# Kernel optimization log

Hardware: AMD Instinct MI355X
Metric: run time of the kernel (lower is better)

Reference implementation:

```python
import jax, jax.numpy as jnp
from jax import lax
import numpy as np

RADIUS = 0.1
NSAMPLE = 32
STRIDE = 3
ED_NSAMPLE = 10


def _sqdist(a, b):
    # a: [B,M,3], b: [B,N,3] -> [B,M,N] squared euclidean distance
    return (jnp.sum(a * a, -1)[:, :, None] + jnp.sum(b * b, -1)[:, None, :]
            - 2.0 * jnp.einsum('bmc,bnc->bmn', a, b))


def setup_inputs() -> dict:
    key = jax.random.key(0)
    ks = jax.random.split(key, 16)
    B, N = 8, 4096
    s = 0.05
    inp = {
        'data': jax.random.normal(ks[0], (B, N, 3), dtype=jnp.float32),
        'numpoints': N,
        # stem MLP 3 -> 64
        'W_stem': jax.random.normal(ks[1], (3, 64), dtype=jnp.float32) * s,
        'b_stem': jnp.zeros((64,), jnp.float32),
        # SA shared MLP (3 dp + 64 fj) -> 128
        'W_sa': jax.random.normal(ks[2], (67, 128), dtype=jnp.float32) * s,
        'b_sa': jnp.zeros((128,), jnp.float32),
        # FP MLP (128 interp + 64 skip) -> 64
        'W_fp': jax.random.normal(ks[3], (192, 64), dtype=jnp.float32) * s,
        'b_fp': jnp.zeros((64,), jnp.float32),
        # eigen-feature MLP 3 -> 4 -> 4
        'W_e1': jax.random.normal(ks[4], (3, 4), dtype=jnp.float32) * s,
        'b_e1': jnp.zeros((4,), jnp.float32),
        'W_e2': jax.random.normal(ks[5], (4, 4), dtype=jnp.float32) * s,
        'b_e2': jnp.zeros((4,), jnp.float32),
        # conv_final 1x1: 68 -> 64, + BN affine
        'W_fin': jax.random.normal(ks[6], (68, 64), dtype=jnp.float32) * s,
        'b_fin': jnp.zeros((64,), jnp.float32),
        'gamma': jnp.ones((64,), jnp.float32),
        'beta': jnp.zeros((64,), jnp.float32),
    }
    return inp


def reference(data, numpoints, W_stem, b_stem, W_sa, b_sa, W_fp, b_fp,
              W_e1, b_e1, W_e2, b_e2, W_fin, b_fin, gamma, beta):
    B, N, _ = data.shape
    b_ix = jnp.arange(B)[:, None, None]

    # ---------- encoder: stem MLP ----------
    f0 = jax.nn.relu(data @ W_stem + b_stem)  # [B,N,64]

    # set abstraction: stride-subsample centers, ball query, dp_fj, MLP, max
    sub_idx = jnp.arange(0, N, STRIDE)
    new_xyz = data[:, sub_idx]                 # [B,M,3]
    d2 = _sqdist(new_xyz, data)                # [B,M,N]
    col = jnp.arange(N, dtype=jnp.int32)
    valid = d2 < RADIUS * RADIUS
    keys = jnp.where(valid, col, N + col)      # first-valid ball query ordering
    negk, _ = lax.top_k(-keys, NSAMPLE)
    idx = -negk                                # [B,M,ns]
    first = idx[..., :1]                       # self point always valid
    idx = jnp.where(idx >= N, first, idx)
    g_xyz = data[b_ix, idx]                    # [B,M,ns,3]
    dp = (g_xyz - new_xyz[:, :, None, :]) / RADIUS  # normalize_dp
    g_f = f0[b_ix, idx]                        # [B,M,ns,64]
    feat = jnp.concatenate([dp, g_f], -1)      # [B,M,ns,67]
    h = jax.nn.relu(feat @ W_sa + b_sa)        # [B,M,ns,128]
    f_sub = jnp.max(h, axis=2)                 # [B,M,128]

    # ---------- decoder: 3-NN inverse-distance feature propagation ----------
    d2f = _sqdist(data, new_xyz)               # [B,N,M]
    negd, nn = lax.top_k(-d2f, 3)
    w = 1.0 / (-negd + 1e-8)
    w = w / jnp.sum(w, -1, keepdims=True)      # [B,N,3]
    nbr_f = f_sub[b_ix, nn]                    # [B,N,3,128]
    interp = jnp.einsum('bnk,bnkc->bnc', w, nbr_f)
    f = jax.nn.relu(jnp.concatenate([interp, f0], -1) @ W_fp + b_fp)  # [B,N,64]

    # ---------- KNN covariance eigen-features ----------
    d2e = _sqdist(data, data)                  # [B,N,N]
    _, gidx = lax.top_k(-d2e, ED_NSAMPLE)      # [B,N,k]
    nbr = data[b_ix, gidx]                     # [B,N,k,3]
    cen = nbr - jnp.mean(nbr, axis=2, keepdims=True)
    cov = jnp.einsum('bnkc,bnkd->bncd', cen, cen) / ED_NSAMPLE  # [B,N,3,3]
    eig = jnp.linalg.eigvalsh(cov)             # [B,N,3] ascending
    ef = jax.nn.relu(eig @ W_e1 + b_e1) @ W_e2 + b_e2  # [B,N,4]

    # ---------- fused 1x1 conv + BN (training-mode stats) + relu ----------
    z_in = jnp.concatenate([f, ef], -1)        # [B,N,68]
    zc = z_in @ W_fin + b_fin                  # [B,N,64]
    mu = jnp.mean(zc, axis=(0, 1))
    var = jnp.var(zc, axis=(0, 1))
    z = jax.nn.relu((zc - mu) * lax.rsqrt(var + 1e-5) * gamma + beta)
    z = jnp.transpose(z, (0, 2, 1))            # [B,64,N]
    return (data, z)
```

## Files before the change

kernel.cpp:

```cpp
#include <hip/hip_runtime.h>
#include <stdint.h>

#define BB 8
#define NN 4096
#define MM 1366
#define NS 32
#define RAD2 0.01f
#define NCH 16
#define CHUNK (NN/NCH)

static_assert(NCH * CHUNK == NN, "chunking");

__device__ __forceinline__ float rl(float v, int l) {
    return __int_as_float(__builtin_amdgcn_readlane(__float_as_int(v), l));
}
__device__ __forceinline__ uint32_t um(uint32_t a, uint32_t b) { return a < b ? a : b; }
__device__ __forceinline__ uint32_t ux(uint32_t a, uint32_t b) { return a > b ? a : b; }
__device__ __forceinline__ uint32_t um3(uint32_t a, uint32_t b, uint32_t c) { return um(um(a, b), c); }

__device__ __forceinline__ void mrg2(uint32_t* kk, uint32_t s0, uint32_t s1) {
    uint32_t n0 = um(kk[0], s0);
    uint32_t n1 = um3(kk[1], ux(kk[0], s0), s1);
    uint32_t n2 = um3(kk[2], ux(kk[1], s0), ux(kk[0], s1));
    uint32_t n3 = um3(kk[3], ux(kk[2], s0), ux(kk[1], s1));
    uint32_t n4 = um3(kk[4], ux(kk[3], s0), ux(kk[2], s1));
    uint32_t n5 = um3(kk[5], ux(kk[4], s0), ux(kk[3], s1));
    uint32_t n6 = um3(kk[6], ux(kk[5], s0), ux(kk[4], s1));
    uint32_t n7 = um3(kk[7], ux(kk[6], s0), ux(kk[5], s1));
    uint32_t n8 = um3(kk[8], ux(kk[7], s0), ux(kk[6], s1));
    uint32_t n9 = um3(kk[9], ux(kk[8], s0), ux(kk[7], s1));
    kk[0]=n0; kk[1]=n1; kk[2]=n2; kk[3]=n3; kk[4]=n4;
    kk[5]=n5; kk[6]=n6; kk[7]=n7; kk[8]=n8; kk[9]=n9;
}

__device__ __forceinline__ void mrg4(uint32_t* kk, uint32_t s0, uint32_t s1,
                                     uint32_t s2, uint32_t s3) {
    uint32_t n0 = um(kk[0], s0);
    uint32_t n1 = um3(kk[1], ux(kk[0], s0), s1);
    uint32_t n2 = um(um3(kk[2], ux(kk[1], s0), ux(kk[0], s1)), s2);
    uint32_t n3 = um3(um3(kk[3], ux(kk[2], s0), ux(kk[1], s1)), ux(kk[0], s2), s3);
    uint32_t n4 = um3(um3(kk[4], ux(kk[3], s0), ux(kk[2], s1)), ux(kk[1], s2), ux(kk[0], s3));
    uint32_t n5 = um3(um3(kk[5], ux(kk[4], s0), ux(kk[3], s1)), ux(kk[2], s2), ux(kk[1], s3));
    uint32_t n6 = um3(um3(kk[6], ux(kk[5], s0), ux(kk[4], s1)), ux(kk[3], s2), ux(kk[2], s3));
    uint32_t n7 = um3(um3(kk[7], ux(kk[6], s0), ux(kk[5], s1)), ux(kk[4], s2), ux(kk[3], s3));
    uint32_t n8 = um3(um3(kk[8], ux(kk[7], s0), ux(kk[6], s1)), ux(kk[5], s2), ux(kk[4], s3));
    uint32_t n9 = um3(um3(kk[9], ux(kk[8], s0), ux(kk[7], s1)), ux(kk[6], s2), ux(kk[5], s3));
    kk[0]=n0; kk[1]=n1; kk[2]=n2; kk[3]=n3; kk[4]=n4;
    kk[5]=n5; kk[6]=n6; kk[7]=n7; kk[8]=n8; kk[9]=n9;
}

__device__ __forceinline__ void srt4(uint32_t& a, uint32_t& b, uint32_t& c, uint32_t& d) {
    uint32_t t0 = um(a, b), t1 = ux(a, b), t2 = um(c, d), t3 = ux(c, d);
    uint32_t s0 = um(t0, t2), m0 = ux(t0, t2), m1 = um(t1, t3), s3 = ux(t1, t3);
    a = s0; b = um(m0, m1); c = ux(m0, m1); d = s3;
}

__global__ __launch_bounds__(256) void k_prep(const float* __restrict__ data,
                                              float* __restrict__ out,
                                              float4* __restrict__ cand4) {
    int t = blockIdx.x * 256 + threadIdx.x;
    float x = data[t * 3], y = data[t * 3 + 1], z = data[t * 3 + 2];
    out[t * 3] = x; out[t * 3 + 1] = y; out[t * 3 + 2] = z;
    cand4[t] = make_float4(x, y, z, x * x + y * y + z * z);
}

__global__ __launch_bounds__(256) void k_stem(const float* __restrict__ data,
                                              const float* __restrict__ Ws,
                                              const float* __restrict__ bs,
                                              float* __restrict__ f0) {
    int t = blockIdx.x * 256 + threadIdx.x;
    int c = t & 63;
    int r = t >> 6;
    const float* d = data + r * 3;
    float acc = bs[c];
    acc = fmaf(d[0], Ws[c], acc);
    acc = fmaf(d[1], Ws[64 + c], acc);
    acc = fmaf(d[2], Ws[128 + c], acc);
    f0[t] = fmaxf(acc, 0.f);
}

__global__ __launch_bounds__(256) void k_sa(const float4* __restrict__ cand4,
                                            const float* __restrict__ data,
                                            const float* __restrict__ f0,
                                            const uint32_t* __restrict__ mrg,
                                            const float* __restrict__ Wsa,
                                            const float* __restrict__ bsa,
                                            float* __restrict__ fsub) {
    __shared__ float2 sW[67 * 64];
    __shared__ int sIdx[4][NS];
    for (int i = threadIdx.x; i < 67 * 64; i += 256) {
        int k = i >> 6, c = i & 63;
        sW[i] = make_float2(Wsa[k * 128 + c], Wsa[k * 128 + 64 + c]);
    }
    __syncthreads();
    int wv = threadIdx.x >> 6, lane = threadIdx.x & 63;
    int gm = blockIdx.x * 4 + wv;
    if (gm >= BB * MM) return;
    int b = gm / MM, m = gm - b * MM;
    const float4* cb4 = cand4 + b * NN;
    const float* db = data + b * NN * 3;
    float4 cen = cb4[3 * m];
    float cx = cen.x, cy = cen.y, cz = cen.z, sa = cen.w;

    int cnt;
    bool fallback;
    {
        float d2l = 1e30f;
        int idxl = 0;
        if (lane < 10) {
            uint32_t key = mrg[lane * (BB * NN) + b * NN + 3 * m];
            idxl = (int)(key & 0xFFFu);
            float4 c = cb4[idxl];
            float dot = fmaf(cz, c.z, fmaf(cy, c.y, cx * c.x));
            d2l = (sa + c.w) - 2.f * dot;
        }
        bool valid = (lane < 10) && (d2l < RAD2);
        unsigned long long mask = __ballot(valid);
        if (valid) sIdx[wv][__popcll(mask & ((1ull << lane) - 1ull))] = idxl;
        cnt = __popcll(mask);
        fallback = rl(d2l, 9) < RAD2 * 1.0005f;
    }
    if (fallback) {
        cnt = 0;
        for (int base = 0; base < NN; base += 64) {
            int n = base + lane;
            float4 c = cb4[n];
            float dot = fmaf(cz, c.z, fmaf(cy, c.y, cx * c.x));
            float d2 = (sa + c.w) - 2.f * dot;
            bool valid = d2 < RAD2;
            unsigned long long mask = __ballot(valid);
            if (valid) {
                int pos = cnt + __popcll(mask & ((1ull << lane) - 1ull));
                if (pos < NS) sIdx[wv][pos] = n;
            }
            cnt += __popcll(mask);
            if (cnt >= NS) break;
        }
    }
    int scnt = cnt < NS ? cnt : NS;

    float cl = lane == 0 ? cx : (lane == 1 ? cy : cz);
    float hb0 = bsa[lane], hb1 = bsa[64 + lane];
    float m0 = 0.f, m1 = 0.f;

    for (int s0 = 0; s0 < scnt; s0 += 4) {
        float fr[4], fr2[4];
        #pragma unroll
        for (int u = 0; u < 4; ++u) {
            int s = s0 + u;
            if (s >= scnt) s = 0;
            int nj = sIdx[wv][s];
            int fb = (b * NN + nj) * 64;
            float v;
            if (lane >= 3) v = f0[fb + lane - 3];
            else           v = (db[nj * 3 + lane] - cl) * 10.0f;
            fr[u] = v;
            fr2[u] = (lane < 3) ? f0[fb + 61 + lane] : 0.f;
        }
        float h0[4], h1[4];
        #pragma unroll
        for (int u = 0; u < 4; ++u) { h0[u] = hb0; h1[u] = hb1; }
        for (int k = 0; k < 64; ++k) {
            float2 w = sW[k * 64 + lane];
            #pragma unroll
            for (int u = 0; u < 4; ++u) {
                float fv = rl(fr[u], k);
                h0[u] = fmaf(fv, w.x, h0[u]);
                h1[u] = fmaf(fv, w.y, h1[u]);
            }
        }
        #pragma unroll
        for (int k = 64; k < 67; ++k) {
            float2 w = sW[k * 64 + lane];
            #pragma unroll
            for (int u = 0; u < 4; ++u) {
                float fv = rl(fr2[u], k - 64);
                h0[u] = fmaf(fv, w.x, h0[u]);
                h1[u] = fmaf(fv, w.y, h1[u]);
            }
        }
        #pragma unroll
        for (int u = 0; u < 4; ++u) {
            m0 = fmaxf(m0, fmaxf(h0[u], 0.f));
            m1 = fmaxf(m1, fmaxf(h1[u], 0.f));
        }
    }
    fsub[gm * 128 + lane] = m0;
    fsub[gm * 128 + 64 + lane] = m1;
}

__global__ __launch_bounds__(256) void k_interp(const float4* __restrict__ cand4,
                                                const float* __restrict__ fsub,
                                                float* __restrict__ itp) {
    __shared__ float4 sC[MM];
    __shared__ float sMD[4][64][3];
    __shared__ int   sMI[4][64][3];
    __shared__ float sWts[64][3];
    __shared__ int   sNbr[64][3];
    int t = threadIdx.x, wv = t >> 6, lane = t & 63;
    int blk = blockIdx.x;
    int b = blk >> 6;
    int pbase = (blk & 63) * 64;
    const float4* cb4 = cand4 + b * NN;
    for (int m = t; m < MM; m += 256) sC[m] = cb4[3 * m];
    __syncthreads();
    int p = pbase + lane;
    float4 pm = cb4[p];
    float px = pm.x, py = pm.y, pz = pm.z, pa = pm.w;
    float d0 = 1e30f, d1 = 1e30f, d2v = 1e30f;
    int n0 = 0, n1 = 0, n2 = 0;
    int ms = wv * 342, me = ms + 342 < MM ? ms + 342 : MM;
    for (int m = ms; m < me; ++m) {
        float4 c = sC[m];
        float dd = (pa + c.w) - 2.f * (px * c.x + py * c.y + pz * c.z);
        if (dd < d2v) {
            if (dd < d1) {
                d2v = d1; n2 = n1;
                if (dd < d0) { d1 = d0; n1 = n0; d0 = dd; n0 = m; }
                else         { d1 = dd; n1 = m; }
            } else { d2v = dd; n2 = m; }
        }
    }
    sMD[wv][lane][0] = d0; sMD[wv][lane][1] = d1; sMD[wv][lane][2] = d2v;
    sMI[wv][lane][0] = n0; sMI[wv][lane][1] = n1; sMI[wv][lane][2] = n2;
    __syncthreads();
    if (wv == 0) {
        d0 = sMD[0][lane][0]; d1 = sMD[0][lane][1]; d2v = sMD[0][lane][2];
        n0 = sMI[0][lane][0]; n1 = sMI[0][lane][1]; n2 = sMI[0][lane][2];
        for (int w = 1; w < 4; ++w) {
            #pragma unroll
            for (int r = 0; r < 3; ++r) {
                float dd = sMD[w][lane][r];
                int mm = sMI[w][lane][r];
                if (dd < d2v) {
                    if (dd < d1) {
                        d2v = d1; n2 = n1;
                        if (dd < d0) { d1 = d0; n1 = n0; d0 = dd; n0 = mm; }
                        else         { d1 = dd; n1 = mm; }
                    } else { d2v = dd; n2 = mm; }
                }
            }
        }
        float w0 = 1.f / (d0 + 1e-8f), w1 = 1.f / (d1 + 1e-8f), w2 = 1.f / (d2v + 1e-8f);
        float ws = w0 + w1 + w2;
        sWts[lane][0] = w0 / ws; sWts[lane][1] = w1 / ws; sWts[lane][2] = w2 / ws;
        sNbr[lane][0] = n0; sNbr[lane][1] = n1; sNbr[lane][2] = n2;
    }
    __syncthreads();
    for (int i = wv * 16; i < wv * 16 + 16; ++i) {
        float a0 = sWts[i][0], a1 = sWts[i][1], a2 = sWts[i][2];
        const float* r0 = fsub + (b * MM + sNbr[i][0]) * 128;
        const float* r1 = fsub + (b * MM + sNbr[i][1]) * 128;
        const float* r2 = fsub + (b * MM + sNbr[i][2]) * 128;
        float v0 = fmaf(a2, r2[lane], fmaf(a1, r1[lane], a0 * r0[lane]));
        float v1 = fmaf(a2, r2[64 + lane], fmaf(a1, r1[64 + lane], a0 * r0[64 + lane]));
        int row = b * NN + pbase + i;
        itp[row * 128 + lane] = v0;
        itp[row * 128 + 64 + lane] = v1;
    }
}

__global__ __launch_bounds__(256) void k_knn_part(const float4* __restrict__ cand4,
                                                  uint32_t* __restrict__ pk) {
    int t = threadIdx.x;
    int blk = blockIdx.x;
    int ch = blk & (NCH - 1);
    int pg = (blk >> 4) & 15;
    int b = blk >> 8;
    const float4* cb = cand4 + b * NN;
    int c0 = ch * CHUNK;
    int p = pg * 256 + t;
    float4 me = cb[p];
    float px = me.x, py = me.y, pz = me.z, pa = me.w;
    uint32_t kk[10];
    #pragma unroll
    for (int r = 0; r < 10; ++r) kk[r] = 0xFFFFFF00u + r;
    for (int j = 0; j < CHUNK; j += 4) {
        float4 ca = cb[c0 + j];
        float4 cbv = cb[c0 + j + 1];
        float4 cc = cb[c0 + j + 2];
        float4 cd = cb[c0 + j + 3];
        float da = fmaxf(fmaf(-2.f, fmaf(pz, ca.z, fmaf(py, ca.y, px * ca.x)), pa + ca.w), 0.f);
        float db_ = fmaxf(fmaf(-2.f, fmaf(pz, cbv.z, fmaf(py, cbv.y, px * cbv.x)), pa + cbv.w), 0.f);
        float dc = fmaxf(fmaf(-2.f, fmaf(pz, cc.z, fmaf(py, cc.y, px * cc.x)), pa + cc.w), 0.f);
        float dd = fmaxf(fmaf(-2.f, fmaf(pz, cd.z, fmaf(py, cd.y, px * cd.x)), pa + cd.w), 0.f);
        uint32_t ka = (__float_as_uint(da) & 0xFFFFF000u) | (uint32_t)(c0 + j);
        uint32_t kb = (__float_as_uint(db_) & 0xFFFFF000u) | (uint32_t)(c0 + j + 1);
        uint32_t kc = (__float_as_uint(dc) & 0xFFFFF000u) | (uint32_t)(c0 + j + 2);
        uint32_t kd = (__float_as_uint(dd) & 0xFFFFF000u) | (uint32_t)(c0 + j + 3);
        srt4(ka, kb, kc, kd);
        mrg4(kk, ka, kb, kc, kd);
    }
    int gp = b * NN + p;
    #pragma unroll
    for (int r = 0; r < 10; ++r)
        pk[(ch * 10 + r) * (BB * NN) + gp] = kk[r];
}

__device__ __forceinline__ void jrot(float& app, float& aqq, float& apq,
                                     float& arp, float& arq) {
    float ap = apq;
    if (fabsf(ap) > 1e-32f) {
        float th = (aqq - app) / (2.f * ap);
        float t = 1.f / (fabsf(th) + sqrtf(th * th + 1.f));
        t = th < 0.f ? -t : t;
        float c = 1.f / sqrtf(t * t + 1.f);
        float s = t * c;
        app = app - t * ap;
        aqq = aqq + t * ap;
        apq = 0.f;
        float rp = arp, rq = arq;
        arp = c * rp - s * rq;
        arq = s * rp + c * rq;
    }
}

__global__ __launch_bounds__(256) void k_knn_eig(const float4* __restrict__ cand4,
                                                 const uint32_t* __restrict__ pk,
                                                 uint32_t* __restrict__ mrg,
                                                 const float* __restrict__ We1,
                                                 const float* __restrict__ be1,
                                                 const float* __restrict__ We2,
                                                 const float* __restrict__ be2,
                                                 float* __restrict__ ef) {
    int t = blockIdx.x * 256 + threadIdx.x;
    int b = t >> 12;
    const float4* cb = cand4 + b * NN;
    uint32_t kk[10];
    #pragma unroll
    for (int r = 0; r < 10; ++r) kk[r] = pk[r * (BB * NN) + t];
    for (int ch = 1; ch < NCH; ++ch) {
        uint32_t s[10];
        #pragma unroll
        for (int r = 0; r < 10; ++r) s[r] = pk[(ch * 10 + r) * (BB * NN) + t];
        mrg4(kk, s[0], s[1], s[2], s[3]);
        mrg4(kk, s[4], s[5], s[6], s[7]);
        mrg2(kk, s[8], s[9]);
    }
    #pragma unroll
    for (int r = 0; r < 10; ++r)
        mrg[r * (BB * NN) + t] = kk[r];
    float xs[10], ys[10], zs[10];
    float mx = 0.f, my = 0.f, mz = 0.f;
    #pragma unroll
    for (int r = 0; r < 10; ++r) {
        int n = (int)(kk[r] & 0xFFFu);
        float4 cr = cb[n];
        xs[r] = cr.x; ys[r] = cr.y; zs[r] = cr.z;
        mx += xs[r]; my += ys[r]; mz += zs[r];
    }
    mx *= 0.1f; my *= 0.1f; mz *= 0.1f;
    float a00 = 0, a01 = 0, a02 = 0, a11 = 0, a12 = 0, a22 = 0;
    #pragma unroll
    for (int r = 0; r < 10; ++r) {
        float x = xs[r] - mx, y = ys[r] - my, z = zs[r] - mz;
        a00 = fmaf(x, x, a00); a01 = fmaf(x, y, a01); a02 = fmaf(x, z, a02);
        a11 = fmaf(y, y, a11); a12 = fmaf(y, z, a12); a22 = fmaf(z, z, a22);
    }
    a00 *= 0.1f; a01 *= 0.1f; a02 *= 0.1f; a11 *= 0.1f; a12 *= 0.1f; a22 *= 0.1f;
    #pragma unroll
    for (int sweep = 0; sweep < 6; ++sweep) {
        jrot(a00, a11, a01, a02, a12);
        jrot(a00, a22, a02, a01, a12);
        jrot(a11, a22, a12, a01, a02);
    }
    float e0 = a00, e1 = a11, e2 = a22, tmp;
    if (e0 > e1) { tmp = e0; e0 = e1; e1 = tmp; }
    if (e1 > e2) { tmp = e1; e1 = e2; e2 = tmp; }
    if (e0 > e1) { tmp = e0; e0 = e1; e1 = tmp; }
    float tt[4];
    #pragma unroll
    for (int i = 0; i < 4; ++i) {
        float v = be1[i];
        v = fmaf(e0, We1[i], v);
        v = fmaf(e1, We1[4 + i], v);
        v = fmaf(e2, We1[8 + i], v);
        tt[i] = fmaxf(v, 0.f);
    }
    #pragma unroll
    for (int i = 0; i < 4; ++i) {
        float v = be2[i];
        v = fmaf(tt[0], We2[i], v);
        v = fmaf(tt[1], We2[4 + i], v);
        v = fmaf(tt[2], We2[8 + i], v);
        v = fmaf(tt[3], We2[12 + i], v);
        ef[t * 4 + i] = v;
    }
}

__global__ __launch_bounds__(256) void k_fp(const float* __restrict__ itp,
                                            const float* __restrict__ f0,
                                            const float* __restrict__ W,
                                            const float* __restrict__ bias,
                                            float* __restrict__ outf) {
    __shared__ float sW[192 * 64];
    for (int i = threadIdx.x; i < 192 * 64; i += 256) sW[i] = W[i];
    __syncthreads();
    int lane = threadIdx.x & 63;
    int wv = threadIdx.x >> 6;
    float bb = bias[lane];
    int rowbase = blockIdx.x * 64 + wv * 16;
    for (int it = 0; it < 4; ++it) {
        int r = rowbase + it * 4;
        float fa[4], fbv[4], fc[4], acc[4];
        #pragma unroll
        for (int u = 0; u < 4; ++u) {
            fa[u]  = itp[(r + u) * 128 + lane];
            fbv[u] = itp[(r + u) * 128 + 64 + lane];
            fc[u]  = f0[(r + u) * 64 + lane];
            acc[u] = bb;
        }
        #pragma unroll
        for (int k = 0; k < 192; ++k) {
            float w = sW[k * 64 + lane];
            #pragma unroll
            for (int u = 0; u < 4; ++u) {
                float fv = k < 64 ? rl(fa[u], k)
                         : (k < 128 ? rl(fbv[u], k - 64) : rl(fc[u], k - 128));
                acc[u] = fmaf(fv, w, acc[u]);
            }
        }
        #pragma unroll
        for (int u = 0; u < 4; ++u)
            outf[(r + u) * 64 + lane] = fmaxf(acc[u], 0.f);
    }
}

__global__ __launch_bounds__(256) void k_fin(const float* __restrict__ fb,
                                             const float* __restrict__ efb,
                                             const float* __restrict__ W,
                                             const float* __restrict__ bias,
                                             float* __restrict__ zc) {
    __shared__ float sW[68 * 64];
    for (int i = threadIdx.x; i < 68 * 64; i += 256) sW[i] = W[i];
    __syncthreads();
    int lane = threadIdx.x & 63;
    int wv = threadIdx.x >> 6;
    float bb = bias[lane];
    int rowbase = blockIdx.x * 64 + wv * 16;
    for (int it = 0; it < 4; ++it) {
        int r = rowbase + it * 4;
        float fa[4], fe[4], acc[4];
        #pragma unroll
        for (int u = 0; u < 4; ++u) {
            fa[u] = fb[(r + u) * 64 + lane];
            fe[u] = (lane < 4) ? efb[(r + u) * 4 + lane] : 0.f;
            acc[u] = bb;
        }
        #pragma unroll
        for (int k = 0; k < 68; ++k) {
            float w = sW[k * 64 + lane];
            #pragma unroll
            for (int u = 0; u < 4; ++u) {
                float fv = k < 64 ? rl(fa[u], k) : rl(fe[u], k - 64);
                acc[u] = fmaf(fv, w, acc[u]);
            }
        }
        #pragma unroll
        for (int u = 0; u < 4; ++u)
            zc[(r + u) * 64 + lane] = acc[u];
    }
}

__global__ __launch_bounds__(256) void k_stats1(const float* __restrict__ zc,
                                                float* __restrict__ pp) {
    int t = threadIdx.x;
    int c = t & 63, r4 = t >> 6;
    float s = 0.f, sq = 0.f;
    int base = blockIdx.x * 512;
    for (int i = 0; i < 128; ++i) {
        float v = zc[(base + i * 4 + r4) * 64 + c];
        s += v;
        sq = fmaf(v, v, sq);
    }
    __shared__ float ls[256], lq[256];
    ls[t] = s; lq[t] = sq;
    __syncthreads();
    if (t < 64) {
        float st = ls[t] + ls[t + 64] + ls[t + 128] + ls[t + 192];
        float qt = lq[t] + lq[t + 64] + lq[t + 128] + lq[t + 192];
        pp[blockIdx.x * 128 + t] = st;
        pp[blockIdx.x * 128 + 64 + t] = qt;
    }
}

__global__ __launch_bounds__(64) void k_stats2(const float* __restrict__ pp,
                                               const float* __restrict__ gamma,
                                               const float* __restrict__ beta,
                                               float* __restrict__ ss) {
    int c = threadIdx.x;
    float s = 0.f, sq = 0.f;
    for (int k = 0; k < 64; ++k) {
        s += pp[k * 128 + c];
        sq += pp[k * 128 + 64 + c];
    }
    const float inv = 1.f / (float)(BB * NN);
    float mu = s * inv;
    float var = sq * inv - mu * mu;
    float sc = gamma[c] / sqrtf(var + 1e-5f);
    ss[c] = sc;
    ss[64 + c] = beta[c] - mu * sc;
}

__global__ __launch_bounds__(256) void k_norm_t(const float* __restrict__ zc,
                                                const float* __restrict__ ss,
                                                float* __restrict__ out) {
    __shared__ float sT[64][65];
    int blk = blockIdx.x;
    int b = blk >> 6;
    int nbase = (blk & 63) * 64;
    int c = threadIdx.x & 63;
    int r4 = threadIdx.x >> 6;
    float sc = ss[c], sh = ss[64 + c];
    #pragma unroll
    for (int i = 0; i < 16; ++i) {
        int nr = i * 4 + r4;
        float v = zc[(b * NN + nbase + nr) * 64 + c];
        sT[nr][c] = fmaxf(fmaf(v, sc, sh), 0.f);
    }
    __syncthreads();
    int nn = threadIdx.x & 63;
    #pragma unroll
    for (int i = 0; i < 16; ++i) {
        int cc = i * 4 + r4;
        out[BB * NN * 3 + (b * 64 + cc) * NN + nbase + nn] = sT[nn][cc];
    }
}

extern "C" void kernel_launch(void* const* d_in, const int* in_sizes, int n_in,
                              void* d_out, int out_size, void* d_ws, size_t ws_size,
                              hipStream_t stream) {
    const float* data = (const float*)d_in[0];
    const float* Wst  = (const float*)d_in[2];
    const float* bst  = (const float*)d_in[3];
    const float* Wsa  = (const float*)d_in[4];
    const float* bsa  = (const float*)d_in[5];
    const float* Wfp  = (const float*)d_in[6];
    const float* bfp  = (const float*)d_in[7];
    const float* We1  = (const float*)d_in[8];
    const float* be1  = (const float*)d_in[9];
    const float* We2  = (const float*)d_in[10];
    const float* be2  = (const float*)d_in[11];
    const float* Wfin = (const float*)d_in[12];
    const float* bfin = (const float*)d_in[13];
    const float* gamma = (const float*)d_in[14];
    const float* beta  = (const float*)d_in[15];
    float* out = (float*)d_out;

    float* f0   = (float*)d_ws;
    float* fsub = f0 + 2097152;
    float* efb  = fsub + 1398784;
    float* zc   = efb + 131072;
    float* ss   = zc + 2097152;
    float* pp   = ss + 128;
    float4* cand4 = (float4*)(pp + 8192);
    uint32_t* mrgb = (uint32_t*)((float*)cand4 + 131072);
    float* itp  = (float*)mrgb + 1310720;
    float* fb   = itp + 4194304;
    uint32_t* pkk = (uint32_t*)itp;

    k_prep<<<(BB * NN) / 256, 256, 0, stream>>>(data, out, cand4);
    k_stem<<<(BB * NN * 64) / 256, 256, 0, stream>>>(data, Wst, bst, f0);
    k_knn_part<<<BB * 16 * NCH, 256, 0, stream>>>(cand4, pkk);
    k_knn_eig<<<(BB * NN) / 256, 256, 0, stream>>>(cand4, pkk, mrgb, We1, be1, We2, be2, efb);
    k_sa<<<(BB * MM + 3) / 4, 256, 0, stream>>>(cand4, data, f0, mrgb, Wsa, bsa, fsub);
    k_interp<<<BB * 64, 256, 0, stream>>>(cand4, fsub, itp);
    k_fp<<<512, 256, 0, stream>>>(itp, f0, Wfp, bfp, fb);
    k_fin<<<512, 256, 0, stream>>>(fb, efb, Wfin, bfin, zc);
    k_stats1<<<64, 256, 0, stream>>>(zc, pp);
    k_stats2<<<1, 64, 0, stream>>>(pp, gamma, beta, ss);
    k_norm_t<<<512, 256, 0, stream>>>(zc, ss, out);
}
```

Baseline: 318.0 us.

## Fuse prep into stem, BN stats into conv_final, and rework KNN merge

Folds the copy-out and float4 candidate packing into the stem kernel and drops the separate prep launch. Computes BatchNorm partial sums inside the final 1x1 conv kernel, which removes the extra pass that reread zc. The second stats kernel now reduces 512 partials with 256 threads. In the KNN partial kernel, the 4-wide sort plus 4-way merge becomes two 2-wide merges with min/max pre-sorting, and a launch bound of 8 blocks per SM is requested to raise occupancy, which may cost register spills.

Result: slower. 340.2 us (+7.0%).

```diff
diff --git a/kernel.cpp b/kernel.cpp
--- a/kernel.cpp
+++ b/kernel.cpp
@@ -49,25 +49,12 @@
     kk[5]=n5; kk[6]=n6; kk[7]=n7; kk[8]=n8; kk[9]=n9;
 }
 
-__device__ __forceinline__ void srt4(uint32_t& a, uint32_t& b, uint32_t& c, uint32_t& d) {
-    uint32_t t0 = um(a, b), t1 = ux(a, b), t2 = um(c, d), t3 = ux(c, d);
-    uint32_t s0 = um(t0, t2), m0 = ux(t0, t2), m1 = um(t1, t3), s3 = ux(t1, t3);
-    a = s0; b = um(m0, m1); c = ux(m0, m1); d = s3;
-}
-
-__global__ __launch_bounds__(256) void k_prep(const float* __restrict__ data,
-                                              float* __restrict__ out,
-                                              float4* __restrict__ cand4) {
-    int t = blockIdx.x * 256 + threadIdx.x;
-    float x = data[t * 3], y = data[t * 3 + 1], z = data[t * 3 + 2];
-    out[t * 3] = x; out[t * 3 + 1] = y; out[t * 3 + 2] = z;
-    cand4[t] = make_float4(x, y, z, x * x + y * y + z * z);
-}
-
 __global__ __launch_bounds__(256) void k_stem(const float* __restrict__ data,
                                               const float* __restrict__ Ws,
                                               const float* __restrict__ bs,
-                                              float* __restrict__ f0) {
+                                              float* __restrict__ f0,
+                                              float* __restrict__ out,
+                                              float4* __restrict__ cand4) {
     int t = blockIdx.x * 256 + threadIdx.x;
     int c = t & 63;
     int r = t >> 6;
@@ -77,6 +64,13 @@
     acc = fmaf(d[1], Ws[64 + c], acc);
     acc = fmaf(d[2], Ws[128 + c], acc);
     f0[t] = fmaxf(acc, 0.f);
+    int tid = threadIdx.x;
+    if (tid < 12) { int o = blockIdx.x * 12 + tid; out[o] = data[o]; }
+    if (tid < 4) {
+        int rr = blockIdx.x * 4 + tid;
+        float x = data[rr * 3], y = data[rr * 3 + 1], z = data[rr * 3 + 2];
+        cand4[rr] = make_float4(x, y, z, x * x + y * y + z * z);
+    }
 }
 
 __global__ __launch_bounds__(256) void k_sa(const float4* __restrict__ cand4,
@@ -260,8 +254,8 @@
     }
 }
 
-__global__ __launch_bounds__(256) void k_knn_part(const float4* __restrict__ cand4,
-                                                  uint32_t* __restrict__ pk) {
+__global__ __launch_bounds__(256, 8) void k_knn_part(const float4* __restrict__ cand4,
+                                                     uint32_t* __restrict__ pk) {
     int t = threadIdx.x;
     int blk = blockIdx.x;
     int ch = blk & (NCH - 1);
@@ -282,14 +276,14 @@
         float4 cd = cb[c0 + j + 3];
         float da = fmaxf(fmaf(-2.f, fmaf(pz, ca.z, fmaf(py, ca.y, px * ca.x)), pa + ca.w), 0.f);
         float db_ = fmaxf(fmaf(-2.f, fmaf(pz, cbv.z, fmaf(py, cbv.y, px * cbv.x)), pa + cbv.w), 0.f);
+        uint32_t ka = (__float_as_uint(da) & 0xFFFFF000u) | (uint32_t)(c0 + j);
+        uint32_t kb = (__float_as_uint(db_) & 0xFFFFF000u) | (uint32_t)(c0 + j + 1);
+        mrg2(kk, um(ka, kb), ux(ka, kb));
         float dc = fmaxf(fmaf(-2.f, fmaf(pz, cc.z, fmaf(py, cc.y, px * cc.x)), pa + cc.w), 0.f);
         float dd = fmaxf(fmaf(-2.f, fmaf(pz, cd.z, fmaf(py, cd.y, px * cd.x)), pa + cd.w), 0.f);
-        uint32_t ka = (__float_as_uint(da) & 0xFFFFF000u) | (uint32_t)(c0 + j);
-        uint32_t kb = (__float_as_uint(db_) & 0xFFFFF000u) | (uint32_t)(c0 + j + 1);
         uint32_t kc = (__float_as_uint(dc) & 0xFFFFF000u) | (uint32_t)(c0 + j + 2);
         uint32_t kd = (__float_as_uint(dd) & 0xFFFFF000u) | (uint32_t)(c0 + j + 3);
-        srt4(ka, kb, kc, kd);
-        mrg4(kk, ka, kb, kc, kd);
+        mrg2(kk, um(kc, kd), ux(kc, kd));
     }
     int gp = b * NN + p;
     #pragma unroll
@@ -430,14 +424,17 @@
                                              const float* __restrict__ efb,
                                              const float* __restrict__ W,
                                              const float* __restrict__ bias,
-                                             float* __restrict__ zc) {
+                                             float* __restrict__ zc,
+                                             float* __restrict__ pp) {
     __shared__ float sW[68 * 64];
+    __shared__ float ls[4][64], lq[4][64];
     for (int i = threadIdx.x; i < 68 * 64; i += 256) sW[i] = W[i];
     __syncthreads();
     int lane = threadIdx.x & 63;
     int wv = threadIdx.x >> 6;
     float bb = bias[lane];
     int rowbase = blockIdx.x * 64 + wv * 16;
+    float psum = 0.f, psq = 0.f;
     for (int it = 0; it < 4; ++it) {
         int r = rowbase + it * 4;
         float fa[4], fe[4], acc[4];
@@ -457,49 +454,47 @@
             }
         }
         #pragma unroll
-        for (int u = 0; u < 4; ++u)
-            zc[(r + u) * 64 + lane] = acc[u];
-    }
-}
-
-__global__ __launch_bounds__(256) void k_stats1(const float* __restrict__ zc,
-                                                float* __restrict__ pp) {
+        for (int u = 0; u < 4; ++u) {
+            float v = acc[u];
+            zc[(r + u) * 64 + lane] = v;
+            psum += v;
+            psq = fmaf(v, v, psq);
+        }
+    }
+    ls[wv][lane] = psum;
+    lq[wv][lane] = psq;
+    __syncthreads();
+    if (threadIdx.x < 64) {
+        int c = threadIdx.x;
+        pp[blockIdx.x * 128 + c]      = ls[0][c] + ls[1][c] + ls[2][c] + ls[3][c];
+        pp[blockIdx.x * 128 + 64 + c] = lq[0][c] + lq[1][c] + lq[2][c] + lq[3][c];
+    }
+}
+
+__global__ __launch_bounds__(256) void k_stats2(const float* __restrict__ pp,
+                                                const float* __restrict__ gamma,
+                                                const float* __restrict__ beta,
+                                                float* __restrict__ ss) {
+    __shared__ float ls[4][64], lq[4][64];
     int t = threadIdx.x;
-    int c = t & 63, r4 = t >> 6;
+    int c = t & 63, q = t >> 6;
     float s = 0.f, sq = 0.f;
-    int base = blockIdx.x * 512;
-    for (int i = 0; i < 128; ++i) {
-        float v = zc[(base + i * 4 + r4) * 64 + c];
-        s += v;
-        sq = fmaf(v, v, sq);
-    }
-    __shared__ float ls[256], lq[256];
-    ls[t] = s; lq[t] = sq;
-    __syncthreads();
-    if (t < 64) {
-        float st = ls[t] + ls[t + 64] + ls[t + 128] + ls[t + 192];
-        float qt = lq[t] + lq[t + 64] + lq[t + 128] + lq[t + 192];
-        pp[blockIdx.x * 128 + t] = st;
-        pp[blockIdx.x * 128 + 64 + t] = qt;
-    }
-}
-
-__global__ __launch_bounds__(64) void k_stats2(const float* __restrict__ pp,
-                                               const float* __restrict__ gamma,
-                                               const float* __restrict__ beta,
-                                               float* __restrict__ ss) {
-    int c = threadIdx.x;
-    float s = 0.f, sq = 0.f;
-    for (int k = 0; k < 64; ++k) {
+    for (int k = q; k < 512; k += 4) {
         s += pp[k * 128 + c];
         sq += pp[k * 128 + 64 + c];
     }
-    const float inv = 1.f / (float)(BB * NN);
-    float mu = s * inv;
-    float var = sq * inv - mu * mu;
-    float sc = gamma[c] / sqrtf(var + 1e-5f);
-    ss[c] = sc;
-    ss[64 + c] = beta[c] - mu * sc;
+    ls[q][c] = s; lq[q][c] = sq;
+    __syncthreads();
+    if (t < 64) {
+        float S = ls[0][c] + ls[1][c] + ls[2][c] + ls[3][c];
+        float Q = lq[0][c] + lq[1][c] + lq[2][c] + lq[3][c];
+        const float inv = 1.f / (float)(BB * NN);
+        float mu = S * inv;
+        float var = Q * inv - mu * mu;
+        float sc = gamma[c] / sqrtf(var + 1e-5f);
+        ss[c] = sc;
+        ss[64 + c] = beta[c] - mu * sc;
+    }
 }
 
 __global__ __launch_bounds__(256) void k_norm_t(const float* __restrict__ zc,
@@ -553,21 +548,19 @@
     float* zc   = efb + 131072;
     float* ss   = zc + 2097152;
     float* pp   = ss + 128;
-    float4* cand4 = (float4*)(pp + 8192);
+    float4* cand4 = (float4*)(pp + 65536);
     uint32_t* mrgb = (uint32_t*)((float*)cand4 + 131072);
     float* itp  = (float*)mrgb + 1310720;
     float* fb   = itp + 4194304;
     uint32_t* pkk = (uint32_t*)itp;
 
-    k_prep<<<(BB * NN) / 256, 256, 0, stream>>>(data, out, cand4);
-    k_stem<<<(BB * NN * 64) / 256, 256, 0, stream>>>(data, Wst, bst, f0);
+    k_stem<<<(BB * NN * 64) / 256, 256, 0, stream>>>(data, Wst, bst, f0, out, cand4);
     k_knn_part<<<BB * 16 * NCH, 256, 0, stream>>>(cand4, pkk);
     k_knn_eig<<<(BB * NN) / 256, 256, 0, stream>>>(cand4, pkk, mrgb, We1, be1, We2, be2, efb);
     k_sa<<<(BB * MM + 3) / 4, 256, 0, stream>>>(cand4, data, f0, mrgb, Wsa, bsa, fsub);
     k_interp<<<BB * 64, 256, 0, stream>>>(cand4, fsub, itp);
     k_fp<<<512, 256, 0, stream>>>(itp, f0, Wfp, bfp, fb);
-    k_fin<<<512, 256, 0, stream>>>(fb, efb, Wfin, bfin, zc);
-    k_stats1<<<64, 256, 0, stream>>>(zc, pp);
-    k_stats2<<<1, 64, 0, stream>>>(pp, gamma, beta, ss);
+    k_fin<<<512, 256, 0, stream>>>(fb, efb, Wfin, bfin, zc, pp);
+    k_stats2<<<1, 256, 0, stream>>>(pp, gamma, beta, ss);
     k_norm_t<<<512, 256, 0, stream>>>(zc, ss, out);
 }
```
